# Kernel tuning notes

Measured on AMD Instinct MI355X. Metric: run time of the kernel, lower is better.

Reference implementation:

```python
import jax, jax.numpy as jnp
import numpy as np

BERT = 178  # BERT_VECTOR_SIZE
WLEN = 20   # letters per word (dim1 = WLEN + BERT)


def _lstm(x, h0, c0, Wih, Whh, bih, bhh):
    """PyTorch-convention LSTM (gate order i,f,g,o). x: [B,T,D] -> outputs [B,T,H]."""
    xg = jnp.einsum('btd,gd->btg', x, Wih) + bih + bhh  # precompute input projections

    def step(carry, xt):
        h, c = carry
        g = xt + h @ Whh.T
        i, f, gg, o = jnp.split(g, 4, axis=-1)
        c = jax.nn.sigmoid(f) * c + jax.nn.sigmoid(i) * jnp.tanh(gg)
        h = jax.nn.sigmoid(o) * jnp.tanh(c)
        return (h, c), h

    _, hs = jax.lax.scan(step, (h0, c0), jnp.swapaxes(xg, 0, 1))
    return jnp.swapaxes(hs, 0, 1)  # [B,T,H]


def setup_inputs() -> dict:
    key = jax.random.key(0)
    ks = jax.random.split(key, 32)
    B, S, L = 32, 64, 50          # batch, sentence_length, number_of_letters
    Hs, Hm, D, O = 128, 256, 128, 32  # secondary_hidden, main_hidden, word_dims, output_size
    NW = B * S
    T = WLEN + BERT
    Din = D + BERT                # sentence LSTM input size = 306
    s = 0.05
    rn = lambda k, sh: jax.random.normal(k, sh, dtype=jnp.float32)
    return {
        'X': rn(ks[0], (B, S, T, L)),
        'h0w': rn(ks[1], (NW, Hs)), 'c0w': rn(ks[2], (NW, Hs)),
        'h0f': rn(ks[3], (B, Hm)), 'c0f': rn(ks[4], (B, Hm)),
        'h0b': rn(ks[5], (B, Hm)), 'c0b': rn(ks[6], (B, Hm)),
        'Wih_w': rn(ks[7], (4 * Hs, L)) * s, 'Whh_w': rn(ks[8], (4 * Hs, Hs)) * s,
        'bih_w': rn(ks[9], (4 * Hs,)) * s, 'bhh_w': rn(ks[10], (4 * Hs,)) * s,
        'Wl': rn(ks[11], (D, Hs)) * s, 'bl': rn(ks[12], (D,)) * s,
        'Wih_f': rn(ks[13], (4 * Hm, Din)) * s, 'Whh_f': rn(ks[14], (4 * Hm, Hm)) * s,
        'bih_f': rn(ks[15], (4 * Hm,)) * s, 'bhh_f': rn(ks[16], (4 * Hm,)) * s,
        'Wih_b': rn(ks[17], (4 * Hm, Din)) * s, 'Whh_b': rn(ks[18], (4 * Hm, Hm)) * s,
        'bih_b': rn(ks[19], (4 * Hm,)) * s, 'bhh_b': rn(ks[20], (4 * Hm,)) * s,
        'Wo': rn(ks[21], (O, 2 * Hm)) * s, 'bo': rn(ks[22], (O,)) * s,
    }


def reference(X, h0w, c0w, h0f, c0f, h0b, c0b,
              Wih_w, Whh_w, bih_w, bhh_w, Wl, bl,
              Wih_f, Whh_f, bih_f, bhh_f,
              Wih_b, Whh_b, bih_b, bhh_b, Wo, bo):
    B, S = X.shape[0], X.shape[1]
    L = X.shape[-1]
    NW = B * S
    Xw = X.reshape(NW, -1, L)            # [NW, WLEN+BERT, L]
    letters = Xw[:, :WLEN, :]            # [NW, WLEN, L]
    bert = Xw[:, -BERT:, 0]              # vectorized replacement of the double loop

    out_w = _lstm(letters, h0w, c0w, Wih_w, Whh_w, bih_w, bhh_w)
    word_rep = out_w[:, -1, :] @ Wl.T + bl        # [NW, D]
    word_rep = jnp.concatenate([word_rep, bert], axis=1)  # [NW, D+BERT]
    sentences = word_rep.reshape(B, S, -1)

    out_f = _lstm(sentences, h0f, c0f, Wih_f, Whh_f, bih_f, bhh_f)
    out_b = _lstm(sentences[:, ::-1, :], h0b, c0b, Wih_b, Whh_b, bih_b, bhh_b)[:, ::-1, :]
    out = jnp.concatenate([out_f, out_b], axis=-1)  # [B, S, 2*Hm]

    words = out.reshape(NW, -1)
    tags = words @ Wo.T + bo
    return jax.nn.softmax(tags, axis=1)
```

## Files before the change

### kernel.cpp

```cpp
#include <hip/hip_runtime.h>
#include <cstdint>
#include <cstddef>

#define DI static __device__ __forceinline__

using half_t  = _Float16;
using half2_t = __attribute__((ext_vector_type(2))) _Float16;
using half8_t = __attribute__((ext_vector_type(8))) _Float16;
using f32x4_t = __attribute__((ext_vector_type(4))) float;

DI uint32_t pack2(float a, float b){ half2_t h; h[0]=(half_t)a; h[1]=(half_t)b; return __builtin_bit_cast(uint32_t,h); }
DI uint16_t f16b(float a){ return __builtin_bit_cast(uint16_t,(half_t)a); }
DI float lo16(uint32_t u){ half2_t h=__builtin_bit_cast(half2_t,u); return (float)h[0]; }
DI float hi16(uint32_t u){ half2_t h=__builtin_bit_cast(half2_t,u); return (float)h[1]; }
DI float fdot2(uint32_t w, uint32_t x, float acc){
  return __builtin_amdgcn_fdot2(__builtin_bit_cast(half2_t,w), __builtin_bit_cast(half2_t,x), acc, false);
}
DI float sigm(float x){ return __builtin_amdgcn_rcpf(1.f + __expf(-x)); }
DI float tanhf_(float x){ return 1.f - 2.f*__builtin_amdgcn_rcpf(__expf(2.f*x)+1.f); }

#define SROW 308
#define HSTR 280
#define ASTR 344

#define N0 32768
#define N1 16384
#define N2 8192
#define N3 512
#define N4 262144
#define N5 327680
#define N6 2048
#define N7 8192
#define NTOT (N0+N1+N2+N3+N4+N5+N6+N7)

__global__ void k_prep(const float* __restrict__ X,
                       const float* __restrict__ Wih_w, const float* __restrict__ Whh_w,
                       const float* __restrict__ bih_w, const float* __restrict__ bhh_w,
                       const float* __restrict__ Wl,
                       const float* __restrict__ Wih_f, const float* __restrict__ Whh_f,
                       const float* __restrict__ bih_f, const float* __restrict__ bhh_f,
                       const float* __restrict__ Wih_b, const float* __restrict__ Whh_b,
                       const float* __restrict__ bih_b, const float* __restrict__ bhh_b,
                       const float* __restrict__ Wo,
                       uint32_t* __restrict__ wWsw, uint32_t* __restrict__ wWxw,
                       uint32_t* __restrict__ wWlf, float* __restrict__ wbsw,
                       uint32_t* __restrict__ wWs, uint32_t* __restrict__ wWihs,
                       float* __restrict__ wbss, uint32_t* __restrict__ wWo)
{
  for (int i = blockIdx.x*blockDim.x + threadIdx.x; i < NTOT; i += gridDim.x*blockDim.x) {
    int id = i;
    if (id < N0) {
      int kp = id & 63, ng = id >> 6;
      int w = ng>>6, g = (ng>>4)&3, jl = ng&15;
      const float* s = Whh_w + (size_t)(g*128 + w*16 + jl)*128 + 2*kp;
      wWsw[id] = pack2(s[0], s[1]);
    } else if ((id -= N0) < N1) {
      int kp = id & 31, ng = id >> 5;
      int w = ng>>6, g = (ng>>4)&3, jl = ng&15;
      if (kp < 25) {
        const float* s = Wih_w + (size_t)(g*128 + w*16 + jl)*50 + 2*kp;
        wWxw[id] = pack2(s[0], s[1]);
      } else wWxw[id] = 0u;
    } else if ((id -= N1) < N2) {
      int kp = id & 63, d = id >> 6;
      const float* s = Wl + (size_t)d*128 + 2*kp;
      wWlf[id] = pack2(s[0], s[1]);
    } else if ((id -= N2) < N3) {
      int g = id & 3, j = id>>2;
      wbsw[id] = bih_w[g*128+j] + bhh_w[g*128+j];
    } else if ((id -= N3) < N4) {
      int kp = id & 127, ng = (id>>7)&1023, dir = id>>17;
      int w = ng>>7, g = (ng>>5)&3, jl = ng&31;
      int row = g*256 + w*32 + jl;
      const float* s = (dir ? Whh_b : Whh_f) + (size_t)row*256 + 2*kp;
      wWs[id] = pack2(s[0], s[1]);
    } else if ((id -= N4) < N5) {
      int kp = id % 160; int q = id / 160;
      int ng = q & 1023, dir = q >> 10;
      int w = ng>>7, g = (ng>>5)&3, jl = ng&31;
      int row = g*256 + w*32 + jl;
      uint32_t v = 0u;
      if (kp < 153) {
        const float* s = (dir ? Wih_b : Wih_f) + (size_t)row*306 + 2*kp;
        v = pack2(s[0], s[1]);
      }
      wWihs[id] = v;
    } else if ((id -= N5) < N6) {
      int g = id & 3, j = (id>>2)&255, dir = id>>10;
      int row = g*256+j;
      wbss[id] = dir ? (bih_b[row]+bhh_b[row]) : (bih_f[row]+bhh_f[row]);
    } else { id -= N6;
      int o = id & 31, kp = id>>5;
      const float* s = Wo + (size_t)o*512 + 2*kp;
      wWo[id] = pack2(s[0], s[1]);
    }
  }
}

__global__ __launch_bounds__(512, 2) void k_word(
    const float* __restrict__ X, const float* __restrict__ h0w, const float* __restrict__ c0w,
    const uint32_t* __restrict__ wWsw, const uint32_t* __restrict__ wWxw,
    const float* __restrict__ wbsw, const uint32_t* __restrict__ wWlf,
    const float* __restrict__ bl, float* __restrict__ sent)
{
  __shared__ __align__(16) uint32_t lets[11520];
  __shared__ __align__(16) uint16_t hbuf[2][2176];
  const int tid = threadIdx.x;
  const int wave = tid >> 6, lane = tid & 63;
  const int l15 = lane & 15, l4 = lane >> 4;
  const int wg0 = blockIdx.x * 16;

  uint4 Bh[4][4], Bx[4][2];
  #pragma unroll
  for (int g = 0; g < 4; ++g) {
    int ng = wave*64 + g*16 + l15;
    #pragma unroll
    for (int Kt = 0; Kt < 4; ++Kt) Bh[g][Kt] = *(const uint4*)(wWsw + ng*64 + Kt*16 + l4*4);
    #pragma unroll
    for (int Kt = 0; Kt < 2; ++Kt) Bx[g][Kt] = *(const uint4*)(wWxw + ng*32 + Kt*16 + l4*4);
  }
  for (int i = tid; i < 16*178; i += 512) {
    int m = i / 178, ii = i - m*178;
    sent[(size_t)(wg0+m)*SROW + 128 + ii] = X[(size_t)(wg0+m)*9900 + (20+ii)*50];
  }
  for (int i = tid; i < 11520; i += 512) {
    int c = i % 36, mt = i / 36; int m = mt & 15, t = mt >> 4;
    lets[i] = (c < 25) ? pack2(X[(size_t)(wg0+m)*9900 + t*50 + 2*c],
                               X[(size_t)(wg0+m)*9900 + t*50 + 2*c + 1]) : 0u;
  }
  for (int i = tid; i < 2048; i += 512) {
    int m = i >> 7, k = i & 127;
    hbuf[0][m*136 + k] = f16b(h0w[(size_t)(wg0+m)*128 + k]);
  }
  const float4 bs = *(const float4*)(wbsw + (wave*16 + l15)*4);
  float cr[4];
  #pragma unroll
  for (int r = 0; r < 4; ++r) cr[r] = c0w[(size_t)(wg0 + l4*4 + r)*128 + wave*16 + l15];
  __syncthreads();

  uint16_t* hc = hbuf[0];
  uint16_t* hn = hbuf[1];
  const uint16_t* lp = (const uint16_t*)lets;
  #pragma unroll 1
  for (int t = 0; t < 20; ++t) {
    f32x4_t acc[4];
    acc[0] = (f32x4_t){bs.x,bs.x,bs.x,bs.x};
    acc[1] = (f32x4_t){bs.y,bs.y,bs.y,bs.y};
    acc[2] = (f32x4_t){bs.z,bs.z,bs.z,bs.z};
    acc[3] = (f32x4_t){bs.w,bs.w,bs.w,bs.w};
    #pragma unroll
    for (int Kt = 0; Kt < 2; ++Kt) {
      uint4 av = *(const uint4*)(lp + (t*16 + l15)*72 + Kt*32 + l4*8);
      half8_t a = __builtin_bit_cast(half8_t, av);
      #pragma unroll
      for (int g = 0; g < 4; ++g)
        acc[g] = __builtin_amdgcn_mfma_f32_16x16x32_f16(a, __builtin_bit_cast(half8_t, Bx[g][Kt]), acc[g], 0,0,0);
    }
    #pragma unroll
    for (int Kt = 0; Kt < 4; ++Kt) {
      uint4 av = *(const uint4*)(hc + l15*136 + Kt*32 + l4*8);
      half8_t a = __builtin_bit_cast(half8_t, av);
      #pragma unroll
      for (int g = 0; g < 4; ++g)
        acc[g] = __builtin_amdgcn_mfma_f32_16x16x32_f16(a, __builtin_bit_cast(half8_t, Bh[g][Kt]), acc[g], 0,0,0);
    }
    #pragma unroll
    for (int r = 0; r < 4; ++r) {
      float cc = sigm(acc[1][r])*cr[r] + sigm(acc[0][r])*tanhf_(acc[2][r]);
      cr[r] = cc;
      float hh = sigm(acc[3][r])*tanhf_(cc);
      hn[(l4*4+r)*136 + wave*16 + l15] = f16b(hh);
    }
    uint16_t* tp = hc; hc = hn; hn = tp;
    __syncthreads();
  }
  uint4 Bl[4];
  #pragma unroll
  for (int Kt = 0; Kt < 4; ++Kt) Bl[Kt] = *(const uint4*)(wWlf + (wave*16 + l15)*64 + Kt*16 + l4*4);
  f32x4_t a2 = (f32x4_t){0.f,0.f,0.f,0.f};
  #pragma unroll
  for (int Kt = 0; Kt < 4; ++Kt) {
    uint4 av = *(const uint4*)(hc + l15*136 + Kt*32 + l4*8);
    a2 = __builtin_amdgcn_mfma_f32_16x16x32_f16(__builtin_bit_cast(half8_t, av),
                                                __builtin_bit_cast(half8_t, Bl[Kt]), a2, 0,0,0);
  }
  const float blv = bl[wave*16 + l15];
  #pragma unroll
  for (int r = 0; r < 4; ++r)
    sent[(size_t)(wg0 + l4*4 + r)*SROW + wave*16 + l15] = a2[r] + blv;
}

__global__ __launch_bounds__(512) void k_sxg(
    const float* __restrict__ sent, const uint32_t* __restrict__ Wihs,
    const float* __restrict__ bss, uint2* __restrict__ xgq)
{
  __shared__ __align__(16) uint16_t xs[32*ASTR];
  const int tid = threadIdx.x;
  const int wave = tid >> 6, lane = tid & 63;
  const int l15 = lane & 15, l4 = lane >> 4;
  const int dir = blockIdx.x >> 6, tt = blockIdx.x & 63;
  const int si = dir ? (63 - tt) : tt;

  for (int i = tid; i < 32*160; i += 512) {
    int kp = i % 160, b = i / 160;
    uint32_t v = 0u;
    if (kp < 153) {
      const float* s = sent + (size_t)(b*64 + si)*SROW + 2*kp;
      v = pack2(s[0], s[1]);
    }
    *(uint32_t*)(xs + b*ASTR + 2*kp) = v;
  }
  __syncthreads();

  f32x4_t acc[2][8];
  #pragma unroll
  for (int Nt = 0; Nt < 8; ++Nt) {
    int g = Nt >> 1, jh = Nt & 1;
    float bv = bss[(dir*256 + wave*32 + jh*16 + l15)*4 + g];
    acc[0][Nt] = (f32x4_t){bv,bv,bv,bv};
    acc[1][Nt] = (f32x4_t){bv,bv,bv,bv};
  }
  const uint32_t* Bb = Wihs + (size_t)(dir*1024 + wave*128)*160 + l15*160 + l4*4;
  #pragma unroll
  for (int Kt = 0; Kt < 10; ++Kt) {
    uint4 av0 = *(const uint4*)(xs + l15*ASTR + Kt*32 + l4*8);
    uint4 av1 = *(const uint4*)(xs + (16 + l15)*ASTR + Kt*32 + l4*8);
    half8_t a0 = __builtin_bit_cast(half8_t, av0);
    half8_t a1 = __builtin_bit_cast(half8_t, av1);
    #pragma unroll
    for (int Nt = 0; Nt < 8; ++Nt) {
      uint4 bv = *(const uint4*)(Bb + (size_t)Nt*16*160 + Kt*16);
      half8_t b = __builtin_bit_cast(half8_t, bv);
      acc[0][Nt] = __builtin_amdgcn_mfma_f32_16x16x32_f16(a0, b, acc[0][Nt], 0,0,0);
      acc[1][Nt] = __builtin_amdgcn_mfma_f32_16x16x32_f16(a1, b, acc[1][Nt], 0,0,0);
    }
  }
  #pragma unroll
  for (int Mt = 0; Mt < 2; ++Mt)
    #pragma unroll
    for (int jh = 0; jh < 2; ++jh)
      #pragma unroll
      for (int r = 0; r < 4; ++r) {
        uint2 v;
        v.x = pack2(acc[Mt][0+jh][r], acc[Mt][2+jh][r]);
        v.y = pack2(acc[Mt][4+jh][r], acc[Mt][6+jh][r]);
        size_t idx = ((((size_t)(dir*64 + tt)*2 + Mt)*8 + wave)*2 + jh)*256 + l15*16 + l4*4 + r;
        xgq[idx] = v;
      }
}

__global__ __launch_bounds__(512, 2) void k_srec(
    const uint32_t* __restrict__ Ws, const float* __restrict__ h0f, const float* __restrict__ c0f,
    const float* __restrict__ h0b, const float* __restrict__ c0b,
    const uint2* __restrict__ xgq, uint16_t* __restrict__ outfb)
{
  extern __shared__ char smem[];
  uint16_t* h16a = (uint16_t*)(smem + 131072);
  uint16_t* h16b = h16a + 16*HSTR;
  const int tid = threadIdx.x;
  const int wave = tid >> 6, lane = tid & 63;
  const int dir = blockIdx.x >> 1, half = blockIdx.x & 1, m0 = half * 16;
  const int l15 = lane & 15, l4 = lane >> 4;

  uint4 Breg[8][6];
  #pragma unroll
  for (int Nt = 0; Nt < 8; ++Nt) {
    #pragma unroll
    for (int Kt = 0; Kt < 8; ++Kt) {
      int ng = wave*128 + Nt*16 + l15;
      uint4 v = *(const uint4*)(Ws + (size_t)(dir*1024 + ng)*128 + Kt*16 + l4*4);
      if (Kt < 6) Breg[Nt][Kt] = v;
      else *(uint4*)(smem + (((wave*16 + Nt*2 + (Kt-6))*64 + lane)*16)) = v;
    }
  }
  {
    const float* h0 = dir ? h0b : h0f;
    for (int i = tid; i < 16*256; i += 512) {
      int m = i >> 8, k = i & 255;
      h16a[m*HSTR + k] = f16b(h0[(size_t)(m0+m)*256 + k]);
    }
  }
  float cr[2][4];
  {
    const float* c0 = dir ? c0b : c0f;
    #pragma unroll
    for (int jh = 0; jh < 2; ++jh)
      #pragma unroll
      for (int r = 0; r < 4; ++r)
        cr[jh][r] = c0[(size_t)(m0 + l4*4 + r)*256 + wave*32 + jh*16 + l15];
  }
  __syncthreads();

  const char* xbase = (const char*)xgq + (size_t)dir*4194304 + half*32768;
  const uint32_t xlane = wave*4096 + l15*128 + l4*32;
  const int s0 = dir ? 63 : 0;
  const int sdelta = dir ? -65536 : 65536;
  const char* obase = (const char*)outfb + (size_t)s0*65536 + half*32768 + dir*16384;
  const uint32_t olane = (l4*4)*512 + wave*64 + l15*2;
  const uint32_t aoff = l15*HSTR + l4*8;

  uint16_t* hc = h16a;
  uint16_t* hn = h16b;

#define UPD1(JH, R, GI, GF, GG, GO) {                                         \
    float eo = __expf(-(GO));                                                 \
    float ef = __expf(-(GF)), ei = __expf(-(GI)), eg = __expf(-2.f*(GG));     \
    float pef = 1.f + ef, pei = 1.f + ei, peg = 1.f + eg;                     \
    float num = cr[JH][R]*pei*peg + (1.f - eg)*pef;                           \
    float cc  = num * __builtin_amdgcn_rcpf(pef*pei*peg);                     \
    cr[JH][R] = cc;                                                           \
    float ec = __expf(-2.f*cc);                                               \
    float hh = (1.f - ec) * __builtin_amdgcn_rcpf((1.f + ec)*(1.f + eo));     \
    uint16_t hb = f16b(hh);                                                   \
    hn[(l4*4+(R))*HSTR + wave*32 + (JH)*16 + l15] = hb;                       \
    *(uint16_t*)(obase + olane + (R)*512 + (JH)*32) = hb;                     \
  }

  uint4 p0 = *(const uint4*)(xbase + xlane);
  uint4 p1 = *(const uint4*)(xbase + xlane + 16);
  uint4 p2 = *(const uint4*)(xbase + xlane + 2048);
  uint4 p3 = *(const uint4*)(xbase + xlane + 2064);

  #pragma unroll 1
  for (int t = 0; t < 64; ++t) {
    f32x4_t acc[8];
    acc[0] = (f32x4_t){lo16(p0.x), lo16(p0.z), lo16(p1.x), lo16(p1.z)};
    acc[2] = (f32x4_t){hi16(p0.x), hi16(p0.z), hi16(p1.x), hi16(p1.z)};
    acc[4] = (f32x4_t){lo16(p0.y), lo16(p0.w), lo16(p1.y), lo16(p1.w)};
    acc[6] = (f32x4_t){hi16(p0.y), hi16(p0.w), hi16(p1.y), hi16(p1.w)};
    acc[1] = (f32x4_t){lo16(p2.x), lo16(p2.z), lo16(p3.x), lo16(p3.z)};
    acc[3] = (f32x4_t){hi16(p2.x), hi16(p2.z), hi16(p3.x), hi16(p3.z)};
    acc[5] = (f32x4_t){lo16(p2.y), lo16(p2.w), lo16(p3.y), lo16(p3.w)};
    acc[7] = (f32x4_t){hi16(p2.y), hi16(p2.w), hi16(p3.y), hi16(p3.w)};

    __builtin_amdgcn_s_setprio(1);
    #pragma unroll
    for (int Kt = 0; Kt < 8; ++Kt) {
      uint4 av = *(const uint4*)(hc + aoff + Kt*32);
      half8_t a = __builtin_bit_cast(half8_t, av);
      #pragma unroll
      for (int g = 0; g < 4; ++g) {
        const int Nt = g*2;
        uint4 bv;
        if (Kt < 6) bv = Breg[Nt][Kt];
        else bv = *(const uint4*)(smem + (((wave*16 + Nt*2 + (Kt-6))*64 + lane)*16));
        acc[Nt] = __builtin_amdgcn_mfma_f32_16x16x32_f16(a, __builtin_bit_cast(half8_t, bv), acc[Nt], 0,0,0);
      }
    }
    __builtin_amdgcn_s_setprio(0);

    #pragma unroll
    for (int Kt = 0; Kt < 8; ++Kt) {
      uint4 av = *(const uint4*)(hc + aoff + Kt*32);
      half8_t a = __builtin_bit_cast(half8_t, av);
      #pragma unroll
      for (int g = 0; g < 4; ++g) {
        const int Nt = g*2 + 1;
        uint4 bv;
        if (Kt < 6) bv = Breg[Nt][Kt];
        else bv = *(const uint4*)(smem + (((wave*16 + Nt*2 + (Kt-6))*64 + lane)*16));
        acc[Nt] = __builtin_amdgcn_mfma_f32_16x16x32_f16(a, __builtin_bit_cast(half8_t, bv), acc[Nt], 0,0,0);
      }
      if (Kt & 1) {
        const int r = Kt >> 1;
        UPD1(0, r, acc[0][r], acc[2][r], acc[4][r], acc[6][r]);
        __builtin_amdgcn_sched_group_barrier(0x008, 8, 0);
        __builtin_amdgcn_sched_group_barrier(0x002, 44, 0);
      }
    }

    p0 = *(const uint4*)(xbase + xlane + 65536);
    p1 = *(const uint4*)(xbase + xlane + 65536 + 16);
    p2 = *(const uint4*)(xbase + xlane + 65536 + 2048);
    p3 = *(const uint4*)(xbase + xlane + 65536 + 2064);

    #pragma unroll
    for (int r = 0; r < 4; ++r)
      UPD1(1, r, acc[1][r], acc[3][r], acc[5][r], acc[7][r]);

    { uint16_t* tp = hc; hc = hn; hn = tp; }
    xbase += 65536;
    obase += sdelta;
    asm volatile("s_waitcnt lgkmcnt(0)\ns_barrier" ::: "memory");
  }
#undef UPD1
}

__global__ __launch_bounds__(256) void k_tags(
    const uint16_t* __restrict__ outfb, const uint32_t* __restrict__ Wo16,
    const float* __restrict__ bo, float* __restrict__ out)
{
  __shared__ uint32_t xr[8*256];
  const int tid = threadIdx.x;
  const int w0 = blockIdx.x * 8;
  const uint32_t* src = (const uint32_t*)outfb;
  for (int i = tid; i < 2048; i += 256) {
    int w = i >> 8, kp = i & 255;
    int widx = w0 + w;
    int s = widx & 63, q = widx >> 6;
    int half = q >> 4, m = q & 15;
    int dir = kp >> 7, wv = (kp >> 4) & 7, jh = (kp >> 3) & 1, l15h = kp & 7;
    xr[i] = src[s*16384 + half*8192 + dir*4096 + m*128 + wv*16 + jh*8 + l15h];
  }
  __syncthreads();
  const int o = tid & 31, w = tid >> 5;
  float a = bo[o];
  for (int kp = 0; kp < 256; ++kp)
    a = fdot2(Wo16[kp*32 + o], xr[w*256 + kp], a);
  float mx = a;
  #pragma unroll
  for (int off = 16; off; off >>= 1) mx = fmaxf(mx, __shfl_xor(mx, off, 32));
  float e = __expf(a - mx);
  float ssum = e;
  #pragma unroll
  for (int off = 16; off; off >>= 1) ssum += __shfl_xor(ssum, off, 32);
  out[(size_t)(w0+w)*32 + o] = e * __builtin_amdgcn_rcpf(ssum);
}

extern "C" void kernel_launch(void* const* d_in, const int* in_sizes, int n_in,
                              void* d_out, int out_size, void* d_ws, size_t ws_size,
                              hipStream_t stream) {
  const float* X     = (const float*)d_in[0];
  const float* h0w   = (const float*)d_in[1];
  const float* c0w   = (const float*)d_in[2];
  const float* h0f   = (const float*)d_in[3];
  const float* c0f   = (const float*)d_in[4];
  const float* h0b   = (const float*)d_in[5];
  const float* c0b   = (const float*)d_in[6];
  const float* Wih_w = (const float*)d_in[7];
  const float* Whh_w = (const float*)d_in[8];
  const float* bih_w = (const float*)d_in[9];
  const float* bhh_w = (const float*)d_in[10];
  const float* Wl    = (const float*)d_in[11];
  const float* bl    = (const float*)d_in[12];
  const float* Wih_f = (const float*)d_in[13];
  const float* Whh_f = (const float*)d_in[14];
  const float* bih_f = (const float*)d_in[15];
  const float* bhh_f = (const float*)d_in[16];
  const float* Wih_b = (const float*)d_in[17];
  const float* Whh_b = (const float*)d_in[18];
  const float* bih_b = (const float*)d_in[19];
  const float* bhh_b = (const float*)d_in[20];
  const float* Wo    = (const float*)d_in[21];
  const float* bo    = (const float*)d_in[22];

  char* ws = (char*)d_ws;
  uint32_t* wWsw  = (uint32_t*)(ws + 0);
  uint32_t* wWxw  = (uint32_t*)(ws + 131072);
  uint32_t* wWlf  = (uint32_t*)(ws + 196608);
  float*    wbsw  = (float*)   (ws + 229376);
  uint32_t* wWs   = (uint32_t*)(ws + 231424);
  uint32_t* wWihs = (uint32_t*)(ws + 1280000);
  float*    wbss  = (float*)   (ws + 2590720);
  uint32_t* wWo   = (uint32_t*)(ws + 2598912);
  float*    sent  = (float*)   (ws + 2631680);
  uint2*    xgq   = (uint2*)   (ws + 5160960);
  uint16_t* outfb = (uint16_t*)(ws + 13549568);

  hipFuncSetAttribute((const void*)k_srec, hipFuncAttributeMaxDynamicSharedMemorySize, 148992);

  k_prep<<<1024, 256, 0, stream>>>(X, Wih_w, Whh_w, bih_w, bhh_w, Wl, Wih_f, Whh_f, bih_f, bhh_f,
                                   Wih_b, Whh_b, bih_b, bhh_b, Wo,
                                   wWsw, wWxw, wWlf, wbsw, wWs, wWihs, wbss, wWo);
  k_word<<<128, 512, 0, stream>>>(X, h0w, c0w, wWsw, wWxw, wbsw, wWlf, bl, sent);
  k_sxg<<<128, 512, 0, stream>>>(sent, wWihs, wbss, xgq);
  k_srec<<<4, 512, 148992, stream>>>(wWs, h0f, c0f, h0b, c0b, xgq, outfb);
  k_tags<<<256, 256, 0, stream>>>(outfb, wWo, bo, (float*)d_out);
}
```

Before: 271.8 us.

## Fuse weight prep into word LSTM kernel with extra prep blocks

Merges the separate weight-packing kernel into the word-LSTM kernel. Blocks 0-127 run the word LSTM and now read and pack their fp32 weights (Whh_w, Wih_w, Wl, biases) straight from the inputs. Blocks 128 and up pack the sentence-LSTM and output weights at the same time. This removes one launch and the serial dependency between prep and the word LSTM. The cost is unvectorised, strided loads when the word blocks pack weights on the fly, and prep blocks competing with word blocks for compute units.

```diff
diff --git a/kernel.cpp b/kernel.cpp
--- a/kernel.cpp
+++ b/kernel.cpp
@@ -23,86 +23,60 @@
 #define HSTR 280
 #define ASTR 344
 
-#define N0 32768
-#define N1 16384
-#define N2 8192
-#define N3 512
-#define N4 262144
-#define N5 327680
-#define N6 2048
-#define N7 8192
-#define NTOT (N0+N1+N2+N3+N4+N5+N6+N7)
-
-__global__ void k_prep(const float* __restrict__ X,
-                       const float* __restrict__ Wih_w, const float* __restrict__ Whh_w,
-                       const float* __restrict__ bih_w, const float* __restrict__ bhh_w,
-                       const float* __restrict__ Wl,
-                       const float* __restrict__ Wih_f, const float* __restrict__ Whh_f,
-                       const float* __restrict__ bih_f, const float* __restrict__ bhh_f,
-                       const float* __restrict__ Wih_b, const float* __restrict__ Whh_b,
-                       const float* __restrict__ bih_b, const float* __restrict__ bhh_b,
-                       const float* __restrict__ Wo,
-                       uint32_t* __restrict__ wWsw, uint32_t* __restrict__ wWxw,
-                       uint32_t* __restrict__ wWlf, float* __restrict__ wbsw,
-                       uint32_t* __restrict__ wWs, uint32_t* __restrict__ wWihs,
-                       float* __restrict__ wbss, uint32_t* __restrict__ wWo)
+#define P4 262144
+#define P5 327680
+#define P6 2048
+#define P7 8192
+#define PTOT (P4+P5+P6+P7)
+
+__global__ __launch_bounds__(512, 2) void k_wp(
+    const float* __restrict__ X, const float* __restrict__ h0w, const float* __restrict__ c0w,
+    const float* __restrict__ Wih_w, const float* __restrict__ Whh_w,
+    const float* __restrict__ bih_w, const float* __restrict__ bhh_w,
+    const float* __restrict__ Wl, const float* __restrict__ bl,
+    const float* __restrict__ Wih_f, const float* __restrict__ Whh_f,
+    const float* __restrict__ Wih_b, const float* __restrict__ Whh_b,
+    const float* __restrict__ bih_f, const float* __restrict__ bhh_f,
+    const float* __restrict__ bih_b, const float* __restrict__ bhh_b,
+    const float* __restrict__ Wo,
+    uint32_t* __restrict__ wWs, uint32_t* __restrict__ wWihs,
+    float* __restrict__ wbss, uint32_t* __restrict__ wWo,
+    float* __restrict__ sent)
 {
-  for (int i = blockIdx.x*blockDim.x + threadIdx.x; i < NTOT; i += gridDim.x*blockDim.x) {
-    int id = i;
-    if (id < N0) {
-      int kp = id & 63, ng = id >> 6;
-      int w = ng>>6, g = (ng>>4)&3, jl = ng&15;
-      const float* s = Whh_w + (size_t)(g*128 + w*16 + jl)*128 + 2*kp;
-      wWsw[id] = pack2(s[0], s[1]);
-    } else if ((id -= N0) < N1) {
-      int kp = id & 31, ng = id >> 5;
-      int w = ng>>6, g = (ng>>4)&3, jl = ng&15;
-      if (kp < 25) {
-        const float* s = Wih_w + (size_t)(g*128 + w*16 + jl)*50 + 2*kp;
-        wWxw[id] = pack2(s[0], s[1]);
-      } else wWxw[id] = 0u;
-    } else if ((id -= N1) < N2) {
-      int kp = id & 63, d = id >> 6;
-      const float* s = Wl + (size_t)d*128 + 2*kp;
-      wWlf[id] = pack2(s[0], s[1]);
-    } else if ((id -= N2) < N3) {
-      int g = id & 3, j = id>>2;
-      wbsw[id] = bih_w[g*128+j] + bhh_w[g*128+j];
-    } else if ((id -= N3) < N4) {
-      int kp = id & 127, ng = (id>>7)&1023, dir = id>>17;
-      int w = ng>>7, g = (ng>>5)&3, jl = ng&31;
-      int row = g*256 + w*32 + jl;
-      const float* s = (dir ? Whh_b : Whh_f) + (size_t)row*256 + 2*kp;
-      wWs[id] = pack2(s[0], s[1]);
-    } else if ((id -= N4) < N5) {
-      int kp = id % 160; int q = id / 160;
-      int ng = q & 1023, dir = q >> 10;
-      int w = ng>>7, g = (ng>>5)&3, jl = ng&31;
-      int row = g*256 + w*32 + jl;
-      uint32_t v = 0u;
-      if (kp < 153) {
-        const float* s = (dir ? Wih_b : Wih_f) + (size_t)row*306 + 2*kp;
-        v = pack2(s[0], s[1]);
-      }
-      wWihs[id] = v;
-    } else if ((id -= N5) < N6) {
-      int g = id & 3, j = (id>>2)&255, dir = id>>10;
-      int row = g*256+j;
-      wbss[id] = dir ? (bih_b[row]+bhh_b[row]) : (bih_f[row]+bhh_f[row]);
-    } else { id -= N6;
-      int o = id & 31, kp = id>>5;
-      const float* s = Wo + (size_t)o*512 + 2*kp;
-      wWo[id] = pack2(s[0], s[1]);
-    }
-  }
-}
-
-__global__ __launch_bounds__(512, 2) void k_word(
-    const float* __restrict__ X, const float* __restrict__ h0w, const float* __restrict__ c0w,
-    const uint32_t* __restrict__ wWsw, const uint32_t* __restrict__ wWxw,
-    const float* __restrict__ wbsw, const uint32_t* __restrict__ wWlf,
-    const float* __restrict__ bl, float* __restrict__ sent)
-{
+  if (blockIdx.x >= 128) {
+    for (int i = (blockIdx.x - 128)*blockDim.x + threadIdx.x; i < PTOT;
+         i += (gridDim.x - 128)*blockDim.x) {
+      int id = i;
+      if (id < P4) {
+        int kp = id & 127, ng = (id>>7)&1023, dir = id>>17;
+        int w = ng>>7, g = (ng>>5)&3, jl = ng&31;
+        int row = g*256 + w*32 + jl;
+        const float* s = (dir ? Whh_b : Whh_f) + (size_t)row*256 + 2*kp;
+        wWs[id] = pack2(s[0], s[1]);
+      } else if ((id -= P4) < P5) {
+        int kp = id % 160; int q = id / 160;
+        int ng = q & 1023, dir = q >> 10;
+        int w = ng>>7, g = (ng>>5)&3, jl = ng&31;
+        int row = g*256 + w*32 + jl;
+        uint32_t v = 0u;
+        if (kp < 153) {
+          const float* s = (dir ? Wih_b : Wih_f) + (size_t)row*306 + 2*kp;
+          v = pack2(s[0], s[1]);
+        }
+        wWihs[id] = v;
+      } else if ((id -= P5) < P6) {
+        int g = id & 3, j = (id>>2)&255, dir = id>>10;
+        int row = g*256+j;
+        wbss[id] = dir ? (bih_b[row]+bhh_b[row]) : (bih_f[row]+bhh_f[row]);
+      } else { id -= P6;
+        int o = id & 31, kp = id>>5;
+        const float* s = Wo + (size_t)o*512 + 2*kp;
+        wWo[id] = pack2(s[0], s[1]);
+      }
+    }
+    return;
+  }
+
   __shared__ __align__(16) uint32_t lets[11520];
   __shared__ __align__(16) uint16_t hbuf[2][2176];
   const int tid = threadIdx.x;
@@ -113,11 +87,34 @@
   uint4 Bh[4][4], Bx[4][2];
   #pragma unroll
   for (int g = 0; g < 4; ++g) {
-    int ng = wave*64 + g*16 + l15;
-    #pragma unroll
-    for (int Kt = 0; Kt < 4; ++Kt) Bh[g][Kt] = *(const uint4*)(wWsw + ng*64 + Kt*16 + l4*4);
-    #pragma unroll
-    for (int Kt = 0; Kt < 2; ++Kt) Bx[g][Kt] = *(const uint4*)(wWxw + ng*32 + Kt*16 + l4*4);
+    const int row = g*128 + wave*16 + l15;
+    #pragma unroll
+    for (int Kt = 0; Kt < 4; ++Kt) {
+      const float* s = Whh_w + (size_t)row*128 + Kt*32 + l4*8;
+      float4 f0 = *(const float4*)s, f1 = *(const float4*)(s + 4);
+      Bh[g][Kt] = make_uint4(pack2(f0.x,f0.y), pack2(f0.z,f0.w),
+                             pack2(f1.x,f1.y), pack2(f1.z,f1.w));
+    }
+    #pragma unroll
+    for (int Kt = 0; Kt < 2; ++Kt) {
+      const int k0 = Kt*32 + l4*8;
+      float v[8];
+      #pragma unroll
+      for (int e = 0; e < 8; ++e) {
+        int k = k0 + e;
+        v[e] = (k < 50) ? Wih_w[(size_t)row*50 + k] : 0.f;
+      }
+      Bx[g][Kt] = make_uint4(pack2(v[0],v[1]), pack2(v[2],v[3]),
+                             pack2(v[4],v[5]), pack2(v[6],v[7]));
+    }
+  }
+  float4 bs;
+  {
+    const int j = wave*16 + l15;
+    bs.x = bih_w[0*128+j] + bhh_w[0*128+j];
+    bs.y = bih_w[1*128+j] + bhh_w[1*128+j];
+    bs.z = bih_w[2*128+j] + bhh_w[2*128+j];
+    bs.w = bih_w[3*128+j] + bhh_w[3*128+j];
   }
   for (int i = tid; i < 16*178; i += 512) {
     int m = i / 178, ii = i - m*178;
@@ -132,7 +129,6 @@
     int m = i >> 7, k = i & 127;
     hbuf[0][m*136 + k] = f16b(h0w[(size_t)(wg0+m)*128 + k]);
   }
-  const float4 bs = *(const float4*)(wbsw + (wave*16 + l15)*4);
   float cr[4];
   #pragma unroll
   for (int r = 0; r < 4; ++r) cr[r] = c0w[(size_t)(wg0 + l4*4 + r)*128 + wave*16 + l15];
@@ -176,7 +172,12 @@
   }
   uint4 Bl[4];
   #pragma unroll
-  for (int Kt = 0; Kt < 4; ++Kt) Bl[Kt] = *(const uint4*)(wWlf + (wave*16 + l15)*64 + Kt*16 + l4*4);
+  for (int Kt = 0; Kt < 4; ++Kt) {
+    const float* s = Wl + (size_t)(wave*16 + l15)*128 + Kt*32 + l4*8;
+    float4 f0 = *(const float4*)s, f1 = *(const float4*)(s + 4);
+    Bl[Kt] = make_uint4(pack2(f0.x,f0.y), pack2(f0.z,f0.w),
+                        pack2(f1.x,f1.y), pack2(f1.z,f1.w));
+  }
   f32x4_t a2 = (f32x4_t){0.f,0.f,0.f,0.f};
   #pragma unroll
   for (int Kt = 0; Kt < 4; ++Kt) {
@@ -445,24 +446,20 @@
   const float* bo    = (const float*)d_in[22];
 
   char* ws = (char*)d_ws;
-  uint32_t* wWsw  = (uint32_t*)(ws + 0);
-  uint32_t* wWxw  = (uint32_t*)(ws + 131072);
-  uint32_t* wWlf  = (uint32_t*)(ws + 196608);
-  float*    wbsw  = (float*)   (ws + 229376);
-  uint32_t* wWs   = (uint32_t*)(ws + 231424);
-  uint32_t* wWihs = (uint32_t*)(ws + 1280000);
-  float*    wbss  = (float*)   (ws + 2590720);
-  uint32_t* wWo   = (uint32_t*)(ws + 2598912);
-  float*    sent  = (float*)   (ws + 2631680);
-  uint2*    xgq   = (uint2*)   (ws + 5160960);
-  uint16_t* outfb = (uint16_t*)(ws + 13549568);
+  uint32_t* wWs   = (uint32_t*)(ws + 0);
+  uint32_t* wWihs = (uint32_t*)(ws + 1048576);
+  float*    wbss  = (float*)   (ws + 2359296);
+  uint32_t* wWo   = (uint32_t*)(ws + 2367488);
+  float*    sent  = (float*)   (ws + 2400256);
+  uint2*    xgq   = (uint2*)   (ws + 4923392);
+  uint16_t* outfb = (uint16_t*)(ws + 13312000);
 
   hipFuncSetAttribute((const void*)k_srec, hipFuncAttributeMaxDynamicSharedMemorySize, 148992);
 
-  k_prep<<<1024, 256, 0, stream>>>(X, Wih_w, Whh_w, bih_w, bhh_w, Wl, Wih_f, Whh_f, bih_f, bhh_f,
-                                   Wih_b, Whh_b, bih_b, bhh_b, Wo,
-                                   wWsw, wWxw, wWlf, wbsw, wWs, wWihs, wbss, wWo);
-  k_word<<<128, 512, 0, stream>>>(X, h0w, c0w, wWsw, wWxw, wbsw, wWlf, bl, sent);
+  k_wp<<<512, 512, 0, stream>>>(X, h0w, c0w, Wih_w, Whh_w, bih_w, bhh_w, Wl, bl,
+                                Wih_f, Whh_f, Wih_b, Whh_b,
+                                bih_f, bhh_f, bih_b, bhh_b, Wo,
+                                wWs, wWihs, wbss, wWo, sent);
   k_sxg<<<128, 512, 0, stream>>>(sent, wWihs, wbss, xgq);
   k_srec<<<4, 512, 148992, stream>>>(wWs, h0f, c0f, h0b, c0b, xgq, outfb);
   k_tags<<<256, 256, 0, stream>>>(outfb, wWo, bo, (float*)d_out);
```

After: 274.4 us. About the same (+1.0%).
